# Kernel optimization log

Hardware: AMD Instinct MI355X
Metric: run time of the kernel (lower is better)

## Reference

```python
import jax, jax.numpy as jnp
import numpy as np
from jax import lax

H = 128  # hidden_size


def lstm_last_h(x, w_ih, w_hh, b_ih, b_hh):
    """PyTorch-style single-layer LSTM; returns final hidden state.
    x: (B, T, D). Gate order i, f, g, o. w_ih: (4H, D), w_hh: (4H, H)."""
    B = x.shape[0]
    Hh = w_hh.shape[1]
    x_proj = jnp.einsum('btd,gd->btg', x, w_ih) + b_ih + b_hh  # (B, T, 4H)

    def step(carry, xt):
        h, c = carry
        gates = xt + h @ w_hh.T
        i, f, g, o = jnp.split(gates, 4, axis=-1)
        i = jax.nn.sigmoid(i)
        f = jax.nn.sigmoid(f)
        g = jnp.tanh(g)
        o = jax.nn.sigmoid(o)
        c = f * c + i * g
        h = o * jnp.tanh(c)
        return (h, c), None

    init = (jnp.zeros((B, Hh), x.dtype), jnp.zeros((B, Hh), x.dtype))
    (h, _), _ = lax.scan(step, init, jnp.swapaxes(x_proj, 0, 1))
    return h  # (B, H)


def setup_inputs() -> dict:
    key = jax.random.key(0)
    ks = jax.random.split(key, 12)
    s = 0.05
    return {
        'x_players': jax.random.normal(ks[0], (64, 22, 128, 2), jnp.float32),
        'x_ball': jax.random.normal(ks[1], (64, 128, 2), jnp.float32),
        'p_w_ih': jax.random.normal(ks[2], (4 * H, 2), jnp.float32) * s,
        'p_w_hh': jax.random.normal(ks[3], (4 * H, H), jnp.float32) * s,
        'p_b_ih': jax.random.normal(ks[4], (4 * H,), jnp.float32) * s,
        'p_b_hh': jax.random.normal(ks[5], (4 * H,), jnp.float32) * s,
        'b_w_ih': jax.random.normal(ks[6], (4 * H, 2), jnp.float32) * s,
        'b_w_hh': jax.random.normal(ks[7], (4 * H, H), jnp.float32) * s,
        'b_b_ih': jax.random.normal(ks[8], (4 * H,), jnp.float32) * s,
        'b_b_hh': jax.random.normal(ks[9], (4 * H,), jnp.float32) * s,
        'fc_w': jax.random.normal(ks[10], (40, 2 * H), jnp.float32) * s,
        'fc_b': jax.random.normal(ks[11], (40,), jnp.float32) * s,
    }


def reference(x_players, x_ball, p_w_ih, p_w_hh, p_b_ih, p_b_hh,
              b_w_ih, b_w_hh, b_b_ih, b_b_hh, fc_w, fc_b):
    B, P, T, D = x_players.shape
    ball_h = lstm_last_h(x_ball, b_w_ih, b_w_hh, b_b_ih, b_b_hh)  # (B, H)
    # Shared player LSTM: fold players into batch (replaces per-player loop).
    ph = lstm_last_h(x_players.reshape(B * P, T, D),
                     p_w_ih, p_w_hh, p_b_ih, p_b_hh).reshape(B, P, H)
    ball_rep = jnp.broadcast_to(ball_h[:, None, :], (B, P, H))
    combined = jnp.concatenate([ph, ball_rep], axis=-1)  # (B, P, 2H)
    out = combined @ fc_w.T + fc_b  # (B, P, 40)
    return out.reshape(B, P, 20, 2)
```

## Files before the change

kernel.cpp:

```cpp
#include <hip/hip_runtime.h>


#define HDIM 128
#define TSTEPS 128
#define NPLAYER 1408
#define NSEQ 1472
#define NB 8
#define NBLK (NSEQ / NB)
#define NPBLK (NPLAYER / NB)
#define KT 5
#define BSTR 168
#define XSTR 258

typedef _Float16 f16x8 __attribute__((ext_vector_type(8)));
typedef _Float16 f16x2 __attribute__((ext_vector_type(2)));
typedef float    f32x4 __attribute__((ext_vector_type(4)));

__device__ __forceinline__ float rcp_fast(float x) { return __builtin_amdgcn_rcpf(x); }
__device__ __forceinline__ float sigmoid_f(float x) { return rcp_fast(1.0f + __expf(-x)); }
__device__ __forceinline__ float tanh_f(float x) {
    return 1.0f - 2.0f * rcp_fast(__expf(2.0f * x) + 1.0f);
}
__device__ __forceinline__ float dpp_xor8(float x) {
    return __int_as_float(__builtin_amdgcn_update_dpp(
        __float_as_int(x), __float_as_int(x), 0x128 , 0xF, 0xF, false));
}

__global__ void __launch_bounds__(512)
__attribute__((amdgpu_waves_per_eu(2, 2)))
lstm_kernel(const float* __restrict__ x_players, const float* __restrict__ x_ball,
            const float* __restrict__ p_w_ih, const float* __restrict__ p_w_hh,
            const float* __restrict__ p_b_ih, const float* __restrict__ p_b_hh,
            const float* __restrict__ b_w_ih, const float* __restrict__ b_w_hh,
            const float* __restrict__ b_b_ih, const float* __restrict__ b_b_hh,
            float* __restrict__ h_all)
{
    const int tid  = threadIdx.x;
    const int blk  = blockIdx.x;
    const int w    = tid >> 6;
    const int lane = tid & 63;
    const int nn   = lane & 15;
    const int q    = lane >> 4;

    const bool ball = (blk >= NPBLK);
    const float* w_ih = ball ? b_w_ih : p_w_ih;
    const float* w_hh = ball ? b_w_hh : p_w_hh;
    const float* bih  = ball ? b_b_ih : p_b_ih;
    const float* bhh  = ball ? b_b_hh : p_b_hh;
    const float* xg   = ball ? (x_ball    + (size_t)(blk - NPBLK) * NB * TSTEPS * 2)
                             : (x_players + (size_t)blk * NB * TSTEPS * 2);

    __shared__ __align__(16) _Float16 b_sh[2][16 * BSTR];
    __shared__ __align__(16) float x_sh[NB * XSTR];

    for (int i = tid; i < NB * 256; i += 512)
        x_sh[(i >> 8) * XSTR + (i & 255)] = xg[i];
    for (int i = tid; i < 2 * 16 * BSTR / 2; i += 512)
        ((int*)b_sh)[i] = 0;

    f16x8 afr[4][KT];
    #pragma unroll
    for (int mi = 0; mi < 4; ++mi) {
        const int r = mi * HDIM + w * 16 + nn;
        const float* wr = w_hh + (size_t)r * HDIM;
        #pragma unroll
        for (int kt = 0; kt < 4; ++kt) {
            const float* p = wr + kt * 32 + q * 8;
            f16x8 a8;
            #pragma unroll
            for (int j = 0; j < 8; ++j) a8[j] = (_Float16)p[j];
            afr[mi][kt] = a8;
        }
        f16x8 a8 = {};
        if (q == 0) {
            a8[0] = (_Float16)w_ih[2 * r];
            a8[1] = (_Float16)w_ih[2 * r + 1];
            a8[2] = (_Float16)(bih[r] + bhh[r]);
        }
        afr[mi][4] = a8;
    }

    const int colh   = nn & 7;
    const int rowoff = (nn < 8) ? 0 : 2;
    const int hrow   = w * 16 + 4 * q + rowoff;
    float c0 = 0.f, c1 = 0.f;

    __syncthreads();
    if (tid < NB) {
        _Float16* br0 = &b_sh[0][tid * BSTR];
        br0[128] = (_Float16)x_sh[tid * XSTR];
        br0[129] = (_Float16)x_sh[tid * XSTR + 1];
        br0[130] = (_Float16)1.0f;
        b_sh[1][tid * BSTR + 130] = (_Float16)1.0f;
    }
    __syncthreads();

    auto substep = [&](int s, const _Float16* bc, _Float16* bn) {
        f16x8 bfr[KT];
        #pragma unroll
        for (int kt = 0; kt < KT; ++kt)
            bfr[kt] = *(const f16x8*)(bc + nn * BSTR + kt * 32 + q * 8);

        f32x4 acc[4];
        #pragma unroll
        for (int mi = 0; mi < 4; ++mi) acc[mi] = (f32x4){0.f, 0.f, 0.f, 0.f};
        #pragma unroll
        for (int kt = 0; kt < KT; ++kt)
            #pragma unroll
            for (int mi = 0; mi < 4; ++mi)
                acc[mi] = __builtin_amdgcn_mfma_f32_16x16x32_f16(afr[mi][kt], bfr[kt], acc[mi], 0, 0, 0);

        if (tid < NB && s + 1 < TSTEPS) {
            const float x0 = x_sh[tid * XSTR + 2 * (s + 1)];
            const float x1 = x_sh[tid * XSTR + 2 * (s + 1) + 1];
            *(f16x2*)&bn[tid * BSTR + 128] = (f16x2){(_Float16)x0, (_Float16)x1};
        }

        float u0[4], u1[4];
        #pragma unroll
        for (int mi = 0; mi < 4; ++mi) {
            const float r2 = dpp_xor8(acc[mi][2]);
            const float r3 = dpp_xor8(acc[mi][3]);
            u0[mi] = (nn < 8) ? acc[mi][0] : r2;
            u1[mi] = (nn < 8) ? acc[mi][1] : r3;
        }
        const float i0 = sigmoid_f(u0[0]), i1 = sigmoid_f(u1[0]);
        const float f0 = sigmoid_f(u0[1]), f1 = sigmoid_f(u1[1]);
        const float g0 = tanh_f(u0[2]),    g1 = tanh_f(u1[2]);
        const float o0 = sigmoid_f(u0[3]), o1 = sigmoid_f(u1[3]);
        c0 = __builtin_fmaf(f0, c0, i0 * g0);
        c1 = __builtin_fmaf(f1, c1, i1 * g1);
        const float h0 = o0 * tanh_f(c0);
        const float h1 = o1 * tanh_f(c1);

        *(f16x2*)&bn[colh * BSTR + hrow] = (f16x2){(_Float16)h0, (_Float16)h1};

        if (s == TSTEPS - 1) {
            float* hp = h_all + (size_t)(blk * NB + colh) * HDIM + hrow;
            hp[0] = h0; hp[1] = h1;
        }
        __syncthreads();
    };

    _Float16* b0 = &b_sh[0][0];
    _Float16* b1 = &b_sh[1][0];
    #pragma unroll 1
    for (int it = 0; it < TSTEPS / 2; ++it) {
        substep(2 * it,     b0, b1);
        substep(2 * it + 1, b1, b0);
        asm volatile("" :
            "+a"(afr[0][0]), "+a"(afr[0][1]), "+a"(afr[0][2]), "+a"(afr[0][3]), "+a"(afr[0][4]),
            "+a"(afr[1][0]), "+a"(afr[1][1]), "+a"(afr[1][2]), "+a"(afr[1][3]), "+a"(afr[1][4]),
            "+a"(afr[2][0]), "+a"(afr[2][1]), "+a"(afr[2][2]), "+a"(afr[2][3]), "+a"(afr[2][4]),
            "+a"(afr[3][0]), "+a"(afr[3][1]), "+a"(afr[3][2]), "+a"(afr[3][3]), "+a"(afr[3][4]));
    }
}

__global__ void __launch_bounds__(64)
fc_kernel(const float* __restrict__ h_all, const float* __restrict__ fc_w,
          const float* __restrict__ fc_b, float* __restrict__ out)
{
    const int blk = blockIdx.x;
    const int b   = blk / 22;
    const int t   = threadIdx.x;

    __shared__ __align__(16) float comb[2 * HDIM];
    for (int i = t; i < HDIM; i += 64) {
        comb[i]        = h_all[(size_t)blk * HDIM + i];
        comb[HDIM + i] = h_all[(size_t)(NPLAYER + b) * HDIM + i];
    }
    __syncthreads();

    if (t < 40) {
        const float* wr = fc_w + (size_t)t * 2 * HDIM;
        float acc = fc_b[t];
        float a1 = 0.0f, a2 = 0.0f, a3 = 0.0f;
        #pragma unroll
        for (int k = 0; k < 2 * HDIM; k += 4) {
            float4 wv = *(const float4*)(wr + k);
            float4 cv = *(const float4*)(comb + k);
            acc = __builtin_fmaf(wv.x, cv.x, acc);
            a1  = __builtin_fmaf(wv.y, cv.y, a1);
            a2  = __builtin_fmaf(wv.z, cv.z, a2);
            a3  = __builtin_fmaf(wv.w, cv.w, a3);
        }
        out[(size_t)blk * 40 + t] = acc + (a1 + a2) + a3;
    }
}

extern "C" void kernel_launch(void* const* d_in, const int* in_sizes, int n_in,
                              void* d_out, int out_size, void* d_ws, size_t ws_size,
                              hipStream_t stream) {
    const float* x_players = (const float*)d_in[0];
    const float* x_ball    = (const float*)d_in[1];
    const float* p_w_ih    = (const float*)d_in[2];
    const float* p_w_hh    = (const float*)d_in[3];
    const float* p_b_ih    = (const float*)d_in[4];
    const float* p_b_hh    = (const float*)d_in[5];
    const float* b_w_ih    = (const float*)d_in[6];
    const float* b_w_hh    = (const float*)d_in[7];
    const float* b_b_ih    = (const float*)d_in[8];
    const float* b_b_hh    = (const float*)d_in[9];
    const float* fc_w      = (const float*)d_in[10];
    const float* fc_b      = (const float*)d_in[11];

    float* h_all = (float*)d_ws;

    lstm_kernel<<<dim3(NBLK), dim3(512), 0, stream>>>(
        x_players, x_ball, p_w_ih, p_w_hh, p_b_ih, p_b_hh,
        b_w_ih, b_w_hh, b_b_ih, b_b_hh, h_all);

    fc_kernel<<<dim3(NPLAYER), dim3(64), 0, stream>>>(
        h_all, fc_w, fc_b, (float*)d_out);
}
```

Measured before the change: 186.7 us.

## Trim LSTM step overheads and batch FC kernel over eight players per block

Several small changes land together. Activations now call exp2 directly with a folded log2e scale. The B-fragment LDS loads run only for the 8 real batch columns, and the shared buffer shrinks to NB rows. The last timestep skips its h write-back and barrier, and the final store moves out of the loop. The FC kernel processes 8 players per 256-thread block instead of one player per 64-thread block, which cuts the launch grid and idle lanes. The risk is that lanes nn>=8 now keep stale bfr values; they are zero-initialized and never reloaded, so this stays correct only because those columns were zero anyway.

```diff
diff --git a/kernel.cpp b/kernel.cpp
--- a/kernel.cpp
+++ b/kernel.cpp
@@ -16,10 +16,14 @@
 typedef _Float16 f16x2 __attribute__((ext_vector_type(2)));
 typedef float    f32x4 __attribute__((ext_vector_type(4)));
 
+#define LOG2E 1.44269504f
+
 __device__ __forceinline__ float rcp_fast(float x) { return __builtin_amdgcn_rcpf(x); }
-__device__ __forceinline__ float sigmoid_f(float x) { return rcp_fast(1.0f + __expf(-x)); }
+__device__ __forceinline__ float sigmoid_f(float x) {
+    return rcp_fast(1.0f + __builtin_amdgcn_exp2f(-LOG2E * x));
+}
 __device__ __forceinline__ float tanh_f(float x) {
-    return 1.0f - 2.0f * rcp_fast(__expf(2.0f * x) + 1.0f);
+    return 1.0f - 2.0f * rcp_fast(__builtin_amdgcn_exp2f(2.0f * LOG2E * x) + 1.0f);
 }
 __device__ __forceinline__ float dpp_xor8(float x) {
     return __int_as_float(__builtin_amdgcn_update_dpp(
@@ -50,12 +54,12 @@
     const float* xg   = ball ? (x_ball    + (size_t)(blk - NPBLK) * NB * TSTEPS * 2)
                              : (x_players + (size_t)blk * NB * TSTEPS * 2);
 
-    __shared__ __align__(16) _Float16 b_sh[2][16 * BSTR];
+    __shared__ __align__(16) _Float16 b_sh[2][NB * BSTR];
     __shared__ __align__(16) float x_sh[NB * XSTR];
 
     for (int i = tid; i < NB * 256; i += 512)
         x_sh[(i >> 8) * XSTR + (i & 255)] = xg[i];
-    for (int i = tid; i < 2 * 16 * BSTR / 2; i += 512)
+    for (int i = tid; i < 2 * NB * BSTR / 2; i += 512)
         ((int*)b_sh)[i] = 0;
 
     f16x8 afr[4][KT];
@@ -84,6 +88,7 @@
     const int rowoff = (nn < 8) ? 0 : 2;
     const int hrow   = w * 16 + 4 * q + rowoff;
     float c0 = 0.f, c1 = 0.f;
+    float h0 = 0.f, h1 = 0.f;
 
     __syncthreads();
     if (tid < NB) {
@@ -95,11 +100,14 @@
     }
     __syncthreads();
 
-    auto substep = [&](int s, const _Float16* bc, _Float16* bn) {
-        f16x8 bfr[KT];
-        #pragma unroll
-        for (int kt = 0; kt < KT; ++kt)
-            bfr[kt] = *(const f16x8*)(bc + nn * BSTR + kt * 32 + q * 8);
+    f16x8 bfr[KT] = {};
+
+    auto substep = [&](int s, const _Float16* bc, _Float16* bn, bool last) {
+        if (nn < 8) {
+            #pragma unroll
+            for (int kt = 0; kt < KT; ++kt)
+                bfr[kt] = *(const f16x8*)(bc + nn * BSTR + kt * 32 + q * 8);
+        }
 
         f32x4 acc[4];
         #pragma unroll
@@ -110,7 +118,7 @@
             for (int mi = 0; mi < 4; ++mi)
                 acc[mi] = __builtin_amdgcn_mfma_f32_16x16x32_f16(afr[mi][kt], bfr[kt], acc[mi], 0, 0, 0);
 
-        if (tid < NB && s + 1 < TSTEPS) {
+        if (!last && tid < NB) {
             const float x0 = x_sh[tid * XSTR + 2 * (s + 1)];
             const float x1 = x_sh[tid * XSTR + 2 * (s + 1) + 1];
             *(f16x2*)&bn[tid * BSTR + 128] = (f16x2){(_Float16)x0, (_Float16)x1};
@@ -130,61 +138,65 @@
         const float o0 = sigmoid_f(u0[3]), o1 = sigmoid_f(u1[3]);
         c0 = __builtin_fmaf(f0, c0, i0 * g0);
         c1 = __builtin_fmaf(f1, c1, i1 * g1);
-        const float h0 = o0 * tanh_f(c0);
-        const float h1 = o1 * tanh_f(c1);
-
-        *(f16x2*)&bn[colh * BSTR + hrow] = (f16x2){(_Float16)h0, (_Float16)h1};
-
-        if (s == TSTEPS - 1) {
-            float* hp = h_all + (size_t)(blk * NB + colh) * HDIM + hrow;
-            hp[0] = h0; hp[1] = h1;
-        }
-        __syncthreads();
+        h0 = o0 * tanh_f(c0);
+        h1 = o1 * tanh_f(c1);
+
+        if (!last) {
+            *(f16x2*)&bn[colh * BSTR + hrow] = (f16x2){(_Float16)h0, (_Float16)h1};
+            __syncthreads();
+        }
     };
 
     _Float16* b0 = &b_sh[0][0];
     _Float16* b1 = &b_sh[1][0];
     #pragma unroll 1
-    for (int it = 0; it < TSTEPS / 2; ++it) {
-        substep(2 * it,     b0, b1);
-        substep(2 * it + 1, b1, b0);
+    for (int it = 0; it < TSTEPS / 2 - 1; ++it) {
+        substep(2 * it,     b0, b1, false);
+        substep(2 * it + 1, b1, b0, false);
         asm volatile("" :
             "+a"(afr[0][0]), "+a"(afr[0][1]), "+a"(afr[0][2]), "+a"(afr[0][3]), "+a"(afr[0][4]),
             "+a"(afr[1][0]), "+a"(afr[1][1]), "+a"(afr[1][2]), "+a"(afr[1][3]), "+a"(afr[1][4]),
             "+a"(afr[2][0]), "+a"(afr[2][1]), "+a"(afr[2][2]), "+a"(afr[2][3]), "+a"(afr[2][4]),
             "+a"(afr[3][0]), "+a"(afr[3][1]), "+a"(afr[3][2]), "+a"(afr[3][3]), "+a"(afr[3][4]));
     }
-}
-
-__global__ void __launch_bounds__(64)
+    substep(126, b0, b1, false);
+    substep(127, b1, b0, true);
+
+    float* hp = h_all + (size_t)(blk * NB + colh) * HDIM + hrow;
+    hp[0] = h0; hp[1] = h1;
+}
+
+__global__ void __launch_bounds__(256)
 fc_kernel(const float* __restrict__ h_all, const float* __restrict__ fc_w,
           const float* __restrict__ fc_b, float* __restrict__ out)
 {
     const int blk = blockIdx.x;
-    const int b   = blk / 22;
-    const int t   = threadIdx.x;
-
-    __shared__ __align__(16) float comb[2 * HDIM];
-    for (int i = t; i < HDIM; i += 64) {
-        comb[i]        = h_all[(size_t)blk * HDIM + i];
-        comb[HDIM + i] = h_all[(size_t)(NPLAYER + b) * HDIM + i];
+    const int tid = threadIdx.x;
+
+    __shared__ __align__(16) float comb[8][2 * HDIM];
+    for (int i = tid; i < 8 * HDIM; i += 256) {
+        const int p = i >> 7, off = i & 127;
+        const int gp = 8 * blk + p;
+        comb[p][off]        = h_all[(size_t)gp * HDIM + off];
+        comb[p][HDIM + off] = h_all[(size_t)(NPLAYER + gp / 22) * HDIM + off];
     }
     __syncthreads();
 
-    if (t < 40) {
-        const float* wr = fc_w + (size_t)t * 2 * HDIM;
-        float acc = fc_b[t];
-        float a1 = 0.0f, a2 = 0.0f, a3 = 0.0f;
+    for (int o = tid; o < 8 * 40; o += 256) {
+        const int p = o / 40, row = o - p * 40;
+        const float* wr = fc_w + (size_t)row * 2 * HDIM;
+        const float* cp = &comb[p][0];
+        float a0 = fc_b[row], a1 = 0.f, a2 = 0.f, a3 = 0.f;
         #pragma unroll
         for (int k = 0; k < 2 * HDIM; k += 4) {
             float4 wv = *(const float4*)(wr + k);
-            float4 cv = *(const float4*)(comb + k);
-            acc = __builtin_fmaf(wv.x, cv.x, acc);
-            a1  = __builtin_fmaf(wv.y, cv.y, a1);
-            a2  = __builtin_fmaf(wv.z, cv.z, a2);
-            a3  = __builtin_fmaf(wv.w, cv.w, a3);
-        }
-        out[(size_t)blk * 40 + t] = acc + (a1 + a2) + a3;
+            float4 cv = *(const float4*)(cp + k);
+            a0 = __builtin_fmaf(wv.x, cv.x, a0);
+            a1 = __builtin_fmaf(wv.y, cv.y, a1);
+            a2 = __builtin_fmaf(wv.z, cv.z, a2);
+            a3 = __builtin_fmaf(wv.w, cv.w, a3);
+        }
+        out[(size_t)(8 * blk + p) * 40 + row] = (a0 + a1) + (a2 + a3);
     }
 }
 
@@ -210,6 +222,6 @@
         x_players, x_ball, p_w_ih, p_w_hh, p_b_ih, p_b_hh,
         b_w_ih, b_w_hh, b_b_ih, b_b_hh, h_all);
 
-    fc_kernel<<<dim3(NPLAYER), dim3(64), 0, stream>>>(
+    fc_kernel<<<dim3(NPBLK), dim3(256), 0, stream>>>(
         h_all, fc_w, fc_b, (float*)d_out);
 }
```

After: 185.4 us. Within noise of the previous version (-0.7%).
